# Performance work log

Hardware: AMD Instinct MI355X
Metric: run time of the kernel (lower is better)

The kernel has to match this reference:

```python
import jax, jax.numpy as jnp
import numpy as np

B, S, H = 4, 8192, 1024


def setup_inputs() -> dict:
    key = jax.random.key(0)
    kq, kk, kv, k1, k2, k3, k4 = jax.random.split(key, 7)
    residual_init_factor = 1.0
    return {
        "q": jax.random.normal(kq, (B, S, H), dtype=jnp.float32),
        "k": jax.random.normal(kk, (B, S, H), dtype=jnp.float32),
        "v": jax.random.normal(kv, (B, S, H), dtype=jnp.float32),
        "w_q": 0.01 * jax.random.normal(k1, (H, H), dtype=jnp.float32),
        "w_k": 0.01 * jax.random.normal(k2, (H, H), dtype=jnp.float32),
        "w_v": 0.01 * jax.random.normal(k3, (H, H), dtype=jnp.float32),
        "w_p": 0.01 * residual_init_factor * jax.random.normal(k4, (H, H), dtype=jnp.float32),
    }


def reference(q, k, v, w_q, w_k, w_v, w_p):
    # Projections: [B,S,H] @ [H,H]
    emb_q = jnp.einsum("bsh,hd->bsd", q, w_q)
    emb_k = jnp.einsum("bsh,hd->bsd", k, w_k)
    emb_v = jnp.einsum("bsh,hd->bsd", v, w_v)
    # AFT-simple: per-channel exponential-weighted causal prefix average
    k_exp = jnp.exp(emb_k)
    k_exp_prefix = jnp.cumsum(k_exp, axis=1)
    k_exp_v_prefix = jnp.cumsum(k_exp * emb_v, axis=1)
    y = jax.nn.sigmoid(emb_q) * (k_exp_v_prefix / k_exp_prefix)
    return jnp.einsum("bsh,hd->bsd", y, w_p)
```

## Files before the change

kernel.cpp:

```cpp
#include <hip/hip_runtime.h>
#include <hip/hip_bf16.h>
#include <cstdint>

#define AS_GLOBAL __attribute__((address_space(1)))
#define AS_LDS    __attribute__((address_space(3)))

typedef __attribute__((ext_vector_type(8))) short bf16x8;
typedef __attribute__((ext_vector_type(8))) unsigned short u16x8;
typedef __attribute__((ext_vector_type(4))) float f32x4;

static __device__ __forceinline__ ushort f2bf(float x) {
    union { float f; uint32_t u; } c;
    c.f = x;
    uint32_t u = c.u;
    u += 0x7fffu + ((u >> 16) & 1u);
    return (ushort)(u >> 16);
}
static __device__ __forceinline__ float bf2f(ushort u) {
    union { uint32_t i; float f; } c;
    c.i = ((uint32_t)u) << 16;
    return c.f;
}

static __device__ __forceinline__ void gload_lds16(const void* g, void* l) {
    __builtin_amdgcn_global_load_lds(
        (const AS_GLOBAL uint32_t*)(uintptr_t)g,
        (AS_LDS uint32_t*)(uint32_t)(uintptr_t)l,
        16, 0, 0);
}

__global__ __launch_bounds__(256)
void cvt_f32_bf16(const float4* __restrict__ in, u16x8* __restrict__ out, int n8) {
    int i = blockIdx.x * 256 + threadIdx.x;
    int stride = gridDim.x * 256;
    for (; i < n8; i += stride) {
        float4 a = in[i * 2], b = in[i * 2 + 1];
        u16x8 o;
        o[0] = f2bf(a.x); o[1] = f2bf(a.y); o[2] = f2bf(a.z); o[3] = f2bf(a.w);
        o[4] = f2bf(b.x); o[5] = f2bf(b.y); o[6] = f2bf(b.z); o[7] = f2bf(b.w);
        out[i] = o;
    }
}

__global__ __launch_bounds__(256)
void transpose_to_bf16(const float* __restrict__ w, ushort* __restrict__ wt, int K, int N) {
    __shared__ float tile[32][33];
    int bn = blockIdx.x * 32;
    int bk = blockIdx.y * 32;
    int tx = threadIdx.x & 31, ty = threadIdx.x >> 5;
    #pragma unroll
    for (int i = 0; i < 32; i += 8)
        tile[ty + i][tx] = w[(size_t)(bk + ty + i) * N + bn + tx];
    __syncthreads();
    #pragma unroll
    for (int i = 0; i < 32; i += 8)
        wt[(size_t)(bn + ty + i) * K + bk + tx] = f2bf(tile[tx][ty + i]);
}

template<int EPI, int OUT_BF>
__global__ __launch_bounds__(256)
void gemm128(const ushort* __restrict__ A, const ushort* __restrict__ Bt,
             void* __restrict__ Cv) {
    constexpr int K = 1024, N = 1024;
    __shared__ ushort sA[3][128 * 32];
    __shared__ ushort sB[3][128 * 32];
    const int tid  = threadIdx.x;
    const int wid  = tid >> 6;
    const int lane = tid & 63;
    const int wr = wid >> 1, wc = wid & 1;
    const int lr = lane & 15;
    const int kb = lane >> 4;

    const int wg = blockIdx.x;
    const int xcd = wg & 7, local = wg >> 3;
    const int bm = xcd * 32 + (local >> 3);
    const int bn = local & 7;
    const int m0 = bm * 128, n0 = bn * 128;

    f32x4 acc[4][4] = {};

    auto stage = [&](int tile, int buf) {
        const int kt0 = tile * 32;
        ushort* dA = &sA[buf][0];
        ushort* dB = &sB[buf][0];
        #pragma unroll
        for (int j = 0; j < 2; j++) {
            int c = j * 256 + tid;
            int r = c >> 2, p = c & 3;
            int s = p ^ ((r >> 1) & 3);
            gload_lds16(A  + (size_t)(m0 + r) * K + kt0 + s * 8, dA + c * 8);
            gload_lds16(Bt + (size_t)(n0 + r) * K + kt0 + s * 8, dB + c * 8);
        }
    };
    auto compute = [&](int buf) {
        const ushort* pA = &sA[buf][0];
        const ushort* pB = &sB[buf][0];
        const int xs = (lr >> 1) & 3;
        bf16x8 af[4], bv[4];
        #pragma unroll
        for (int m = 0; m < 4; m++)
            af[m] = *(const bf16x8*)&pA[(wr * 64 + m * 16 + lr) * 32 + (kb ^ xs) * 8];
        #pragma unroll
        for (int n = 0; n < 4; n++)
            bv[n] = *(const bf16x8*)&pB[(wc * 64 + n * 16 + lr) * 32 + (kb ^ xs) * 8];
        #pragma unroll
        for (int m = 0; m < 4; m++)
            #pragma unroll
            for (int n = 0; n < 4; n++)
                acc[m][n] = __builtin_amdgcn_mfma_f32_16x16x32_bf16(af[m], bv[n], acc[m][n], 0, 0, 0);
    };

    stage(0, 0);
    stage(1, 1);
    asm volatile("s_waitcnt vmcnt(4)" ::: "memory");
    __builtin_amdgcn_s_barrier();
    asm volatile("" ::: "memory");

    for (int t = 0; t < 32; t++) {
        const int bc = t % 3;
        if (t < 30) stage(t + 2, (t + 2) % 3);
        compute(bc);
        if (t < 30)      asm volatile("s_waitcnt vmcnt(4)" ::: "memory");
        else if (t == 30) asm volatile("s_waitcnt vmcnt(0)" ::: "memory");
        asm volatile("s_waitcnt lgkmcnt(0)" ::: "memory");
        __builtin_amdgcn_s_barrier();
        asm volatile("" ::: "memory");
    }

    float*  Cf = (float*)Cv;
    ushort* Cb = (ushort*)Cv;
    #pragma unroll
    for (int m = 0; m < 4; m++) {
        #pragma unroll
        for (int n = 0; n < 4; n++) {
            #pragma unroll
            for (int r = 0; r < 4; r++) {
                int row = m0 + wr * 64 + m * 16 + (lane >> 4) * 4 + r;
                int col = n0 + wc * 64 + n * 16 + (lane & 15);
                float v = acc[m][n][r];
                if (EPI == 1) v = 1.0f / (1.0f + __expf(-v));
                else if (EPI == 2) v = __expf(v);
                size_t idx = (size_t)row * N + col;
                if (OUT_BF) Cb[idx] = f2bf(v);
                else        Cf[idx] = v;
            }
        }
    }
}

__global__ __launch_bounds__(256)
void scan_partials(const ushort* __restrict__ ke, const ushort* __restrict__ ev,
                   float* __restrict__ pke, float* __restrict__ pkv) {
    const int H = 1024, S = 8192, CHUNK = 32, BH = 4096;
    int c  = blockIdx.x * 2 + (threadIdx.x >> 7);
    int h0 = (threadIdx.x & 127) * 8;
    int b  = blockIdx.y;
    size_t base = ((size_t)b * S + (size_t)c * CHUNK) * H + h0;
    float se[8] = {}, sv[8] = {};
    for (int s = 0; s < CHUNK; s++) {
        u16x8 e8 = *(const u16x8*)(ke + base + (size_t)s * H);
        u16x8 v8 = *(const u16x8*)(ev + base + (size_t)s * H);
        #pragma unroll
        for (int i = 0; i < 8; i++) {
            float e = bf2f(e8[i]);
            se[i] += e;
            sv[i] += e * bf2f(v8[i]);
        }
    }
    size_t p = (size_t)c * BH + b * H + h0;
    *(float4*)(pke + p)     = make_float4(se[0], se[1], se[2], se[3]);
    *(float4*)(pke + p + 4) = make_float4(se[4], se[5], se[6], se[7]);
    *(float4*)(pkv + p)     = make_float4(sv[0], sv[1], sv[2], sv[3]);
    *(float4*)(pkv + p + 4) = make_float4(sv[4], sv[5], sv[6], sv[7]);
}

__global__ __launch_bounds__(256)
void scan_offsets(float* __restrict__ pke, float* __restrict__ pkv, int nch, int BH) {
    int i = blockIdx.x * blockDim.x + threadIdx.x;
    if (i >= BH) return;
    float rke = 0.f, rkv = 0.f;
    for (int c = 0; c < nch; c++) {
        size_t idx = (size_t)c * BH + i;
        float a = pke[idx], b = pkv[idx];
        pke[idx] = rke; pkv[idx] = rkv;
        rke += a; rkv += b;
    }
}

__global__ __launch_bounds__(256)
void scan_final(const ushort* __restrict__ ke, const ushort* __restrict__ ev,
                const ushort* __restrict__ sq,
                const float* __restrict__ pke, const float* __restrict__ pkv,
                ushort* __restrict__ ybf) {
    const int H = 1024, S = 8192, CHUNK = 32, BH = 4096;
    int c  = blockIdx.x * 2 + (threadIdx.x >> 7);
    int h0 = (threadIdx.x & 127) * 8;
    int b  = blockIdx.y;
    size_t p = (size_t)c * BH + b * H + h0;
    float rke[8], rkv[8];
    *(float4*)(rke)     = *(const float4*)(pke + p);
    *(float4*)(rke + 4) = *(const float4*)(pke + p + 4);
    *(float4*)(rkv)     = *(const float4*)(pkv + p);
    *(float4*)(rkv + 4) = *(const float4*)(pkv + p + 4);
    size_t base = ((size_t)b * S + (size_t)c * CHUNK) * H + h0;
    for (int s = 0; s < CHUNK; s++) {
        size_t idx = base + (size_t)s * H;
        u16x8 e8 = *(const u16x8*)(ke + idx);
        u16x8 v8 = *(const u16x8*)(ev + idx);
        u16x8 q8 = *(const u16x8*)(sq + idx);
        u16x8 o;
        #pragma unroll
        for (int i = 0; i < 8; i++) {
            float e = bf2f(e8[i]);
            rke[i] += e;
            rkv[i] += e * bf2f(v8[i]);
            o[i] = f2bf(bf2f(q8[i]) * (rkv[i] / rke[i]));
        }
        *(u16x8*)(ybf + idx) = o;
    }
}

extern "C" void kernel_launch(void* const* d_in, const int* in_sizes, int n_in,
                              void* d_out, int out_size, void* d_ws, size_t ws_size,
                              hipStream_t stream) {
    const float* q   = (const float*)d_in[0];
    const float* k   = (const float*)d_in[1];
    const float* v   = (const float*)d_in[2];
    const float* w_q = (const float*)d_in[3];
    const float* w_k = (const float*)d_in[4];
    const float* w_v = (const float*)d_in[5];
    const float* w_p = (const float*)d_in[6];
    float* out = (float*)d_out;

    const int B = 4, S = 8192, H = 1024;
    const int M = B * S;
    const size_t MH = (size_t)M * H;
    const int NCH = 256;
    const int BH = B * H;

    char* ws = (char*)d_ws;
    size_t off = 0;
    auto alloc = [&](size_t bytes) -> char* {
        char* p = ws + off;
        off += (bytes + 255) & ~(size_t)255;
        return p;
    };
    ushort* abuf = (ushort*)alloc(MH * 2);
    ushort* wqt  = (ushort*)alloc((size_t)H * H * 2);
    ushort* wkt  = (ushort*)alloc((size_t)H * H * 2);
    ushort* wvt  = (ushort*)alloc((size_t)H * H * 2);
    ushort* wpt  = (ushort*)alloc((size_t)H * H * 2);
    ushort* sqb  = (ushort*)alloc(MH * 2);
    ushort* keb  = (ushort*)alloc(MH * 2);
    ushort* evb  = (ushort*)alloc(MH * 2);
    float*  pke  = (float*)alloc((size_t)NCH * BH * 4);
    float*  pkv  = (float*)alloc((size_t)NCH * BH * 4);

    dim3 tg(H / 32, H / 32);
    const int ngg = (M / 128) * (H / 128);
    dim3 gs(NCH / 2, B);
    const int n8 = (int)(MH / 8);

    transpose_to_bf16<<<tg, 256, 0, stream>>>(w_q, wqt, H, H);
    transpose_to_bf16<<<tg, 256, 0, stream>>>(w_k, wkt, H, H);
    transpose_to_bf16<<<tg, 256, 0, stream>>>(w_v, wvt, H, H);
    transpose_to_bf16<<<tg, 256, 0, stream>>>(w_p, wpt, H, H);

    cvt_f32_bf16<<<2048, 256, 0, stream>>>((const float4*)q, (u16x8*)abuf, n8);
    gemm128<1, 1><<<ngg, 256, 0, stream>>>(abuf, wqt, sqb);
    cvt_f32_bf16<<<2048, 256, 0, stream>>>((const float4*)k, (u16x8*)abuf, n8);
    gemm128<2, 1><<<ngg, 256, 0, stream>>>(abuf, wkt, keb);
    cvt_f32_bf16<<<2048, 256, 0, stream>>>((const float4*)v, (u16x8*)abuf, n8);
    gemm128<0, 1><<<ngg, 256, 0, stream>>>(abuf, wvt, evb);

    scan_partials<<<gs, 256, 0, stream>>>(keb, evb, pke, pkv);
    scan_offsets<<<BH / 256, 256, 0, stream>>>(pke, pkv, NCH, BH);
    scan_final<<<gs, 256, 0, stream>>>(keb, evb, sqb, pke, pkv, abuf);

    gemm128<0, 0><<<ngg, 256, 0, stream>>>(abuf, wpt, out);
}
```

Before: 584.3 us.

## Fuse fp32-to-bf16 input conversion into projection GEMM loads; batch weight transposes

The three projection GEMMs now read fp32 activations straight into LDS through a swizzled layout and convert them to bf16 while building MFMA fragments. This drops the separate conversion kernels and their bf16 round trip through memory. The four weight transposes are merged into a single launch indexed by blockIdx.z. In exchange, the fp32 path needs twice the A-tile LDS, is cut to double buffering with a full vmcnt(0) wait each iteration, and adds conversion ALU work inside the main loop.

```diff
diff --git a/kernel.cpp b/kernel.cpp
--- a/kernel.cpp
+++ b/kernel.cpp
@@ -30,21 +30,19 @@
 }
 
 __global__ __launch_bounds__(256)
-void cvt_f32_bf16(const float4* __restrict__ in, u16x8* __restrict__ out, int n8) {
-    int i = blockIdx.x * 256 + threadIdx.x;
-    int stride = gridDim.x * 256;
-    for (; i < n8; i += stride) {
-        float4 a = in[i * 2], b = in[i * 2 + 1];
-        u16x8 o;
-        o[0] = f2bf(a.x); o[1] = f2bf(a.y); o[2] = f2bf(a.z); o[3] = f2bf(a.w);
-        o[4] = f2bf(b.x); o[5] = f2bf(b.y); o[6] = f2bf(b.z); o[7] = f2bf(b.w);
-        out[i] = o;
-    }
-}
-
-__global__ __launch_bounds__(256)
-void transpose_to_bf16(const float* __restrict__ w, ushort* __restrict__ wt, int K, int N) {
+void transpose4_to_bf16(const float* __restrict__ w0, const float* __restrict__ w1,
+                        const float* __restrict__ w2, const float* __restrict__ w3,
+                        ushort* __restrict__ t0, ushort* __restrict__ t1,
+                        ushort* __restrict__ t2, ushort* __restrict__ t3) {
+    const int K = 1024, N = 1024;
     __shared__ float tile[32][33];
+    const float* w; ushort* wt;
+    switch (blockIdx.z) {
+        case 0: w = w0; wt = t0; break;
+        case 1: w = w1; wt = t1; break;
+        case 2: w = w2; wt = t2; break;
+        default: w = w3; wt = t3; break;
+    }
     int bn = blockIdx.x * 32;
     int bk = blockIdx.y * 32;
     int tx = threadIdx.x & 31, ty = threadIdx.x >> 5;
@@ -57,13 +55,15 @@
         wt[(size_t)(bn + ty + i) * K + bk + tx] = f2bf(tile[tx][ty + i]);
 }
 
-template<int EPI, int OUT_BF>
-__global__ __launch_bounds__(256)
-void gemm128(const ushort* __restrict__ A, const ushort* __restrict__ Bt,
+template<int EPI, int A_F32, int OUT_BF>
+__global__ __launch_bounds__(256)
+void gemm128(const void* __restrict__ Av, const ushort* __restrict__ Bt,
              void* __restrict__ Cv) {
     constexpr int K = 1024, N = 1024;
-    __shared__ ushort sA[3][128 * 32];
-    __shared__ ushort sB[3][128 * 32];
+    constexpr int A_TUS = A_F32 ? 8192 : 4096;
+    constexpr int DEPTH = A_F32 ? 2 : 3;
+    __shared__ alignas(16) ushort sA[DEPTH * A_TUS];
+    __shared__ alignas(16) ushort sB[DEPTH * 4096];
     const int tid  = threadIdx.x;
     const int wid  = tid >> 6;
     const int lane = tid & 63;
@@ -77,29 +77,70 @@
     const int bn = local & 7;
     const int m0 = bm * 128, n0 = bn * 128;
 
+    const float*  Af = (const float*)Av;
+    const ushort* Ab = (const ushort*)Av;
+
     f32x4 acc[4][4] = {};
 
-    auto stage = [&](int tile, int buf) {
+    auto stageA = [&](int tile, int buf) {
         const int kt0 = tile * 32;
-        ushort* dA = &sA[buf][0];
-        ushort* dB = &sB[buf][0];
+        if constexpr (A_F32) {
+            float* dst = (float*)&sA[buf * A_TUS];
+            #pragma unroll
+            for (int j = 0; j < 4; j++) {
+                int c = j * 256 + tid;
+                int r = c >> 3, p = c & 7;
+                int s = p ^ (r & 7);
+                gload_lds16(Af + (size_t)(m0 + r) * K + kt0 + s * 4, dst + c * 4);
+            }
+        } else {
+            ushort* dst = &sA[buf * A_TUS];
+            #pragma unroll
+            for (int j = 0; j < 2; j++) {
+                int c = j * 256 + tid;
+                int r = c >> 2, p = c & 3;
+                int s = p ^ ((r >> 1) & 3);
+                gload_lds16(Ab + (size_t)(m0 + r) * K + kt0 + s * 8, dst + c * 8);
+            }
+        }
+    };
+    auto stageBf = [&](int tile, int buf) {
+        ushort* dst = &sB[buf * 4096];
+        const int kt0 = tile * 32;
         #pragma unroll
         for (int j = 0; j < 2; j++) {
             int c = j * 256 + tid;
             int r = c >> 2, p = c & 3;
             int s = p ^ ((r >> 1) & 3);
-            gload_lds16(A  + (size_t)(m0 + r) * K + kt0 + s * 8, dA + c * 8);
-            gload_lds16(Bt + (size_t)(n0 + r) * K + kt0 + s * 8, dB + c * 8);
+            gload_lds16(Bt + (size_t)(n0 + r) * K + kt0 + s * 8, dst + c * 8);
         }
     };
     auto compute = [&](int buf) {
-        const ushort* pA = &sA[buf][0];
-        const ushort* pB = &sB[buf][0];
+        bf16x8 af[4], bv[4];
         const int xs = (lr >> 1) & 3;
-        bf16x8 af[4], bv[4];
-        #pragma unroll
-        for (int m = 0; m < 4; m++)
-            af[m] = *(const bf16x8*)&pA[(wr * 64 + m * 16 + lr) * 32 + (kb ^ xs) * 8];
+        if constexpr (A_F32) {
+            const float* pAf = (const float*)&sA[buf * A_TUS];
+            #pragma unroll
+            for (int m = 0; m < 4; m++) {
+                int r = wr * 64 + m * 16 + lr;
+                int q0 = (2 * kb) ^ (r & 7);
+                int q1 = (2 * kb + 1) ^ (r & 7);
+                f32x4 a0 = *(const f32x4*)&pAf[r * 32 + q0 * 4];
+                f32x4 a1 = *(const f32x4*)&pAf[r * 32 + q1 * 4];
+                bf16x8 t;
+                t[0]=(short)f2bf(a0[0]); t[1]=(short)f2bf(a0[1]);
+                t[2]=(short)f2bf(a0[2]); t[3]=(short)f2bf(a0[3]);
+                t[4]=(short)f2bf(a1[0]); t[5]=(short)f2bf(a1[1]);
+                t[6]=(short)f2bf(a1[2]); t[7]=(short)f2bf(a1[3]);
+                af[m] = t;
+            }
+        } else {
+            const ushort* pA = &sA[buf * A_TUS];
+            #pragma unroll
+            for (int m = 0; m < 4; m++)
+                af[m] = *(const bf16x8*)&pA[(wr * 64 + m * 16 + lr) * 32 + (kb ^ xs) * 8];
+        }
+        const ushort* pB = &sB[buf * 4096];
         #pragma unroll
         for (int n = 0; n < 4; n++)
             bv[n] = *(const bf16x8*)&pB[(wc * 64 + n * 16 + lr) * 32 + (kb ^ xs) * 8];
@@ -110,21 +151,35 @@
                 acc[m][n] = __builtin_amdgcn_mfma_f32_16x16x32_bf16(af[m], bv[n], acc[m][n], 0, 0, 0);
     };
 
-    stage(0, 0);
-    stage(1, 1);
-    asm volatile("s_waitcnt vmcnt(4)" ::: "memory");
-    __builtin_amdgcn_s_barrier();
-    asm volatile("" ::: "memory");
-
-    for (int t = 0; t < 32; t++) {
-        const int bc = t % 3;
-        if (t < 30) stage(t + 2, (t + 2) % 3);
-        compute(bc);
-        if (t < 30)      asm volatile("s_waitcnt vmcnt(4)" ::: "memory");
-        else if (t == 30) asm volatile("s_waitcnt vmcnt(0)" ::: "memory");
-        asm volatile("s_waitcnt lgkmcnt(0)" ::: "memory");
+    if constexpr (A_F32) {
+        stageA(0, 0); stageBf(0, 0);
+        asm volatile("s_waitcnt vmcnt(0)" ::: "memory");
         __builtin_amdgcn_s_barrier();
         asm volatile("" ::: "memory");
+        for (int t = 0; t < 32; t++) {
+            if (t < 31) { stageA(t + 1, (t + 1) & 1); stageBf(t + 1, (t + 1) & 1); }
+            compute(t & 1);
+            if (t < 31) asm volatile("s_waitcnt vmcnt(0)" ::: "memory");
+            asm volatile("s_waitcnt lgkmcnt(0)" ::: "memory");
+            __builtin_amdgcn_s_barrier();
+            asm volatile("" ::: "memory");
+        }
+    } else {
+        stageA(0, 0); stageBf(0, 0);
+        stageA(1, 1); stageBf(1, 1);
+        asm volatile("s_waitcnt vmcnt(4)" ::: "memory");
+        __builtin_amdgcn_s_barrier();
+        asm volatile("" ::: "memory");
+        for (int t = 0; t < 32; t++) {
+            const int bc = t % 3;
+            if (t < 30) { int b2 = (t + 2) % 3; stageA(t + 2, b2); stageBf(t + 2, b2); }
+            compute(bc);
+            if (t < 30)       asm volatile("s_waitcnt vmcnt(4)" ::: "memory");
+            else if (t == 30) asm volatile("s_waitcnt vmcnt(0)" ::: "memory");
+            asm volatile("s_waitcnt lgkmcnt(0)" ::: "memory");
+            __builtin_amdgcn_s_barrier();
+            asm volatile("" ::: "memory");
+        }
     }
 
     float*  Cf = (float*)Cv;
@@ -245,7 +300,7 @@
         off += (bytes + 255) & ~(size_t)255;
         return p;
     };
-    ushort* abuf = (ushort*)alloc(MH * 2);
+    ushort* ybuf = (ushort*)alloc(MH * 2);
     ushort* wqt  = (ushort*)alloc((size_t)H * H * 2);
     ushort* wkt  = (ushort*)alloc((size_t)H * H * 2);
     ushort* wvt  = (ushort*)alloc((size_t)H * H * 2);
@@ -256,26 +311,19 @@
     float*  pke  = (float*)alloc((size_t)NCH * BH * 4);
     float*  pkv  = (float*)alloc((size_t)NCH * BH * 4);
 
-    dim3 tg(H / 32, H / 32);
     const int ngg = (M / 128) * (H / 128);
+    dim3 tg(H / 32, H / 32, 4);
     dim3 gs(NCH / 2, B);
-    const int n8 = (int)(MH / 8);
-
-    transpose_to_bf16<<<tg, 256, 0, stream>>>(w_q, wqt, H, H);
-    transpose_to_bf16<<<tg, 256, 0, stream>>>(w_k, wkt, H, H);
-    transpose_to_bf16<<<tg, 256, 0, stream>>>(w_v, wvt, H, H);
-    transpose_to_bf16<<<tg, 256, 0, stream>>>(w_p, wpt, H, H);
-
-    cvt_f32_bf16<<<2048, 256, 0, stream>>>((const float4*)q, (u16x8*)abuf, n8);
-    gemm128<1, 1><<<ngg, 256, 0, stream>>>(abuf, wqt, sqb);
-    cvt_f32_bf16<<<2048, 256, 0, stream>>>((const float4*)k, (u16x8*)abuf, n8);
-    gemm128<2, 1><<<ngg, 256, 0, stream>>>(abuf, wkt, keb);
-    cvt_f32_bf16<<<2048, 256, 0, stream>>>((const float4*)v, (u16x8*)abuf, n8);
-    gemm128<0, 1><<<ngg, 256, 0, stream>>>(abuf, wvt, evb);
+
+    transpose4_to_bf16<<<tg, 256, 0, stream>>>(w_q, w_k, w_v, w_p, wqt, wkt, wvt, wpt);
+
+    gemm128<1, 1, 1><<<ngg, 256, 0, stream>>>(q, wqt, sqb);
+    gemm128<2, 1, 1><<<ngg, 256, 0, stream>>>(k, wkt, keb);
+    gemm128<0, 1, 1><<<ngg, 256, 0, stream>>>(v, wvt, evb);
 
     scan_partials<<<gs, 256, 0, stream>>>(keb, evb, pke, pkv);
     scan_offsets<<<BH / 256, 256, 0, stream>>>(pke, pkv, NCH, BH);
-    scan_final<<<gs, 256, 0, stream>>>(keb, evb, sqb, pke, pkv, abuf);
-
-    gemm128<0, 0><<<ngg, 256, 0, stream>>>(abuf, wpt, out);
-}
+    scan_final<<<gs, 256, 0, stream>>>(keb, evb, sqb, pke, pkv, ybuf);
+
+    gemm128<0, 0, 0><<<ngg, 256, 0, stream>>>(ybuf, wpt, out);
+}
```

Measured after the change: 737.7 us. +26.2%, slower.

## Enlarge GEMM tile to 256x128 and batch conversion and transpose launches

Applied to the files above, without the earlier changes.

The GEMM block tile doubles along M (256x128, 8x4 MFMA accumulators per wave). This raises arithmetic intensity per LDS stage and halves the number of workgroups, with the XCD mapping adjusted to match. The three activation conversions and the four weight transposes are each merged into one launch, and separate bf16 buffers are allocated per input. In exchange, register and LDS pressure rise (launch bounds ask for 2 blocks) and the grid shrinks to 1024 blocks.

```diff
diff --git a/kernel.cpp b/kernel.cpp
--- a/kernel.cpp
+++ b/kernel.cpp
@@ -30,7 +30,16 @@
 }
 
 __global__ __launch_bounds__(256)
-void cvt_f32_bf16(const float4* __restrict__ in, u16x8* __restrict__ out, int n8) {
+void cvt3_f32_bf16(const float4* __restrict__ in0, const float4* __restrict__ in1,
+                   const float4* __restrict__ in2,
+                   u16x8* __restrict__ o0, u16x8* __restrict__ o1, u16x8* __restrict__ o2,
+                   int n8) {
+    const float4* in; u16x8* out;
+    switch (blockIdx.y) {
+        case 0: in = in0; out = o0; break;
+        case 1: in = in1; out = o1; break;
+        default: in = in2; out = o2; break;
+    }
     int i = blockIdx.x * 256 + threadIdx.x;
     int stride = gridDim.x * 256;
     for (; i < n8; i += stride) {
@@ -43,8 +52,19 @@
 }
 
 __global__ __launch_bounds__(256)
-void transpose_to_bf16(const float* __restrict__ w, ushort* __restrict__ wt, int K, int N) {
+void transpose4_to_bf16(const float* __restrict__ w0, const float* __restrict__ w1,
+                        const float* __restrict__ w2, const float* __restrict__ w3,
+                        ushort* __restrict__ t0, ushort* __restrict__ t1,
+                        ushort* __restrict__ t2, ushort* __restrict__ t3) {
+    const int K = 1024, N = 1024;
     __shared__ float tile[32][33];
+    const float* w; ushort* wt;
+    switch (blockIdx.z) {
+        case 0: w = w0; wt = t0; break;
+        case 1: w = w1; wt = t1; break;
+        case 2: w = w2; wt = t2; break;
+        default: w = w3; wt = t3; break;
+    }
     int bn = blockIdx.x * 32;
     int bk = blockIdx.y * 32;
     int tx = threadIdx.x & 31, ty = threadIdx.x >> 5;
@@ -58,53 +78,59 @@
 }
 
 template<int EPI, int OUT_BF>
-__global__ __launch_bounds__(256)
-void gemm128(const ushort* __restrict__ A, const ushort* __restrict__ Bt,
-             void* __restrict__ Cv) {
+__global__ __launch_bounds__(256, 2)
+void gemm256x128(const ushort* __restrict__ A, const ushort* __restrict__ Bt,
+                 void* __restrict__ Cv) {
     constexpr int K = 1024, N = 1024;
-    __shared__ ushort sA[3][128 * 32];
-    __shared__ ushort sB[3][128 * 32];
+    __shared__ alignas(16) ushort sA[3 * 8192];
+    __shared__ alignas(16) ushort sB[3 * 4096];
     const int tid  = threadIdx.x;
     const int wid  = tid >> 6;
     const int lane = tid & 63;
     const int wr = wid >> 1, wc = wid & 1;
     const int lr = lane & 15;
     const int kb = lane >> 4;
+    const int xs = (lr >> 1) & 3;
 
     const int wg = blockIdx.x;
     const int xcd = wg & 7, local = wg >> 3;
-    const int bm = xcd * 32 + (local >> 3);
+    const int bm = xcd * 16 + (local >> 3);
     const int bn = local & 7;
-    const int m0 = bm * 128, n0 = bn * 128;
-
-    f32x4 acc[4][4] = {};
+    const int m0 = bm * 256, n0 = bn * 128;
+
+    f32x4 acc[8][4] = {};
 
     auto stage = [&](int tile, int buf) {
         const int kt0 = tile * 32;
-        ushort* dA = &sA[buf][0];
-        ushort* dB = &sB[buf][0];
+        ushort* dA = &sA[buf * 8192];
+        ushort* dB = &sB[buf * 4096];
+        #pragma unroll
+        for (int j = 0; j < 4; j++) {
+            int c = j * 256 + tid;
+            int r = c >> 2, p = c & 3;
+            int s = p ^ ((r >> 1) & 3);
+            gload_lds16(A + (size_t)(m0 + r) * K + kt0 + s * 8, dA + c * 8);
+        }
         #pragma unroll
         for (int j = 0; j < 2; j++) {
             int c = j * 256 + tid;
             int r = c >> 2, p = c & 3;
             int s = p ^ ((r >> 1) & 3);
-            gload_lds16(A  + (size_t)(m0 + r) * K + kt0 + s * 8, dA + c * 8);
             gload_lds16(Bt + (size_t)(n0 + r) * K + kt0 + s * 8, dB + c * 8);
         }
     };
     auto compute = [&](int buf) {
-        const ushort* pA = &sA[buf][0];
-        const ushort* pB = &sB[buf][0];
-        const int xs = (lr >> 1) & 3;
-        bf16x8 af[4], bv[4];
-        #pragma unroll
-        for (int m = 0; m < 4; m++)
-            af[m] = *(const bf16x8*)&pA[(wr * 64 + m * 16 + lr) * 32 + (kb ^ xs) * 8];
+        const ushort* pA = &sA[buf * 8192];
+        const ushort* pB = &sB[buf * 4096];
+        bf16x8 af[8], bv[4];
+        #pragma unroll
+        for (int m = 0; m < 8; m++)
+            af[m] = *(const bf16x8*)&pA[(wr * 128 + m * 16 + lr) * 32 + (kb ^ xs) * 8];
         #pragma unroll
         for (int n = 0; n < 4; n++)
             bv[n] = *(const bf16x8*)&pB[(wc * 64 + n * 16 + lr) * 32 + (kb ^ xs) * 8];
         #pragma unroll
-        for (int m = 0; m < 4; m++)
+        for (int m = 0; m < 8; m++)
             #pragma unroll
             for (int n = 0; n < 4; n++)
                 acc[m][n] = __builtin_amdgcn_mfma_f32_16x16x32_bf16(af[m], bv[n], acc[m][n], 0, 0, 0);
@@ -112,15 +138,14 @@
 
     stage(0, 0);
     stage(1, 1);
-    asm volatile("s_waitcnt vmcnt(4)" ::: "memory");
+    asm volatile("s_waitcnt vmcnt(6)" ::: "memory");
     __builtin_amdgcn_s_barrier();
     asm volatile("" ::: "memory");
 
     for (int t = 0; t < 32; t++) {
-        const int bc = t % 3;
         if (t < 30) stage(t + 2, (t + 2) % 3);
-        compute(bc);
-        if (t < 30)      asm volatile("s_waitcnt vmcnt(4)" ::: "memory");
+        compute(t % 3);
+        if (t < 30)       asm volatile("s_waitcnt vmcnt(6)" ::: "memory");
         else if (t == 30) asm volatile("s_waitcnt vmcnt(0)" ::: "memory");
         asm volatile("s_waitcnt lgkmcnt(0)" ::: "memory");
         __builtin_amdgcn_s_barrier();
@@ -130,12 +155,12 @@
     float*  Cf = (float*)Cv;
     ushort* Cb = (ushort*)Cv;
     #pragma unroll
-    for (int m = 0; m < 4; m++) {
+    for (int m = 0; m < 8; m++) {
         #pragma unroll
         for (int n = 0; n < 4; n++) {
             #pragma unroll
             for (int r = 0; r < 4; r++) {
-                int row = m0 + wr * 64 + m * 16 + (lane >> 4) * 4 + r;
+                int row = m0 + wr * 128 + m * 16 + (lane >> 4) * 4 + r;
                 int col = n0 + wc * 64 + n * 16 + (lane & 15);
                 float v = acc[m][n][r];
                 if (EPI == 1) v = 1.0f / (1.0f + __expf(-v));
@@ -245,7 +270,9 @@
         off += (bytes + 255) & ~(size_t)255;
         return p;
     };
-    ushort* abuf = (ushort*)alloc(MH * 2);
+    ushort* qb   = (ushort*)alloc(MH * 2);
+    ushort* kb_  = (ushort*)alloc(MH * 2);
+    ushort* vb   = (ushort*)alloc(MH * 2);
     ushort* wqt  = (ushort*)alloc((size_t)H * H * 2);
     ushort* wkt  = (ushort*)alloc((size_t)H * H * 2);
     ushort* wvt  = (ushort*)alloc((size_t)H * H * 2);
@@ -256,26 +283,25 @@
     float*  pke  = (float*)alloc((size_t)NCH * BH * 4);
     float*  pkv  = (float*)alloc((size_t)NCH * BH * 4);
 
-    dim3 tg(H / 32, H / 32);
-    const int ngg = (M / 128) * (H / 128);
+    const int ngg = (M / 256) * (H / 128);
+    dim3 tg(H / 32, H / 32, 4);
     dim3 gs(NCH / 2, B);
+    dim3 gc(2048, 3);
     const int n8 = (int)(MH / 8);
 
-    transpose_to_bf16<<<tg, 256, 0, stream>>>(w_q, wqt, H, H);
-    transpose_to_bf16<<<tg, 256, 0, stream>>>(w_k, wkt, H, H);
-    transpose_to_bf16<<<tg, 256, 0, stream>>>(w_v, wvt, H, H);
-    transpose_to_bf16<<<tg, 256, 0, stream>>>(w_p, wpt, H, H);
-
-    cvt_f32_bf16<<<2048, 256, 0, stream>>>((const float4*)q, (u16x8*)abuf, n8);
-    gemm128<1, 1><<<ngg, 256, 0, stream>>>(abuf, wqt, sqb);
-    cvt_f32_bf16<<<2048, 256, 0, stream>>>((const float4*)k, (u16x8*)abuf, n8);
-    gemm128<2, 1><<<ngg, 256, 0, stream>>>(abuf, wkt, keb);
-    cvt_f32_bf16<<<2048, 256, 0, stream>>>((const float4*)v, (u16x8*)abuf, n8);
-    gemm128<0, 1><<<ngg, 256, 0, stream>>>(abuf, wvt, evb);
+    transpose4_to_bf16<<<tg, 256, 0, stream>>>(w_q, w_k, w_v, w_p, wqt, wkt, wvt, wpt);
+
+    cvt3_f32_bf16<<<gc, 256, 0, stream>>>((const float4*)q, (const float4*)k,
+                                          (const float4*)v,
+                                          (u16x8*)qb, (u16x8*)kb_, (u16x8*)vb, n8);
+
+    gemm256x128<1, 1><<<ngg, 256, 0, stream>>>(qb,  wqt, sqb);
+    gemm256x128<2, 1><<<ngg, 256, 0, stream>>>(kb_, wkt, keb);
+    gemm256x128<0, 1><<<ngg, 256, 0, stream>>>(vb,  wvt, evb);
 
     scan_partials<<<gs, 256, 0, stream>>>(keb, evb, pke, pkv);
     scan_offsets<<<BH / 256, 256, 0, stream>>>(pke, pkv, NCH, BH);
-    scan_final<<<gs, 256, 0, stream>>>(keb, evb, sqb, pke, pkv, abuf);
-
-    gemm128<0, 0><<<ngg, 256, 0, stream>>>(abuf, wpt, out);
-}
+    scan_final<<<gs, 256, 0, stream>>>(keb, evb, sqb, pke, pkv, qb);
+
+    gemm256x128<0, 0><<<ngg, 256, 0, stream>>>(qb, wpt, out);
+}
```

Result: slower. 600.3 us (+2.7%).
